# Optimization experiments

Measured on AMD Instinct MI355X. Metric: run time of the kernel, lower is better.

Reference implementation:

```python
import jax, jax.numpy as jnp
import numpy as np

# dims: n=batch, T=n_shifts, dX=16, dU=8, H=256 hidden, L=128 ldim, K=64 n_aux (L=2K)

def setup_inputs() -> dict:
    key = jax.random.key(0)
    ks = jax.random.split(key, 16)
    n, T, dX, dU, H, L, K = 64, 64, 16, 8, 256, 128, 64
    def lin(k, fan_in, shape):
        return (jax.random.uniform(k, shape, jnp.float32) * 2.0 - 1.0) / np.sqrt(fan_in)
    xs = jax.random.normal(ks[0], (n, T, dX), jnp.float32)
    us = jax.random.normal(ks[1], (n, T - 1, dU), jnp.float32)
    theta = jax.random.uniform(ks[2], (K,), jnp.float32) * (2.0 * np.pi)
    inp = {
        'xs': xs, 'us': us,
        # stacked x-aux encoders (K copies): BN affine, 3 linear layers (last no bias), output scale
        'x_gamma': jnp.ones((K, dX)), 'x_beta': jnp.zeros((K, dX)),
        'xW1': lin(ks[3], dX, (K, dX, H)), 'xb1': jnp.zeros((K, H)),
        'xW2': lin(ks[4], H, (K, H, H)), 'xb2': jnp.zeros((K, H)),
        'xW3': lin(ks[5], H, (K, H, L)), 'x_scale': jnp.ones((K, L)),
        # stacked u-aux encoders (K copies)
        'u_gamma': jnp.ones((K, dU)), 'u_beta': jnp.zeros((K, dU)),
        'uW1': lin(ks[6], dU, (K, dU, H)), 'ub1': jnp.zeros((K, H)),
        'uW2': lin(ks[7], H, (K, H, H)), 'ub2': jnp.zeros((K, H)),
        'uW3': lin(ks[8], H, (K, H, L)), 'u_scale': jnp.ones((K, L)),
        # Jordan-block complex eigenvalues (|lam| ~ 0.95)
        'reL': 0.95 * jnp.cos(theta), 'imL': 0.95 * jnp.sin(theta),
        # decoder C: Linear(ldim, dim, bias=False) -> weight [dX, L]
        'C_W': lin(ks[9], L, (dX, L)),
    }
    return inp


def _encoder(x, gamma, beta, W1, b1, W2, b2, W3, scale):
    # x: [M, D]; stacked params over K nets. BN stats (training mode) are per-feature over M,
    # identical across nets since the same x feeds every net.
    mu = x.mean(0)
    var = ((x - mu) ** 2).mean(0)
    xn = (x - mu) * jax.lax.rsqrt(var + 1e-5)          # [M, D]
    h = xn[None] * gamma[:, None, :] + beta[:, None, :]  # [K, M, D]
    h = jax.nn.leaky_relu(jnp.einsum('kmd,kdh->kmh', h, W1) + b1[:, None, :])
    h = jax.nn.leaky_relu(jnp.einsum('kmd,kdh->kmh', h, W2) + b2[:, None, :])
    h = jnp.einsum('kmd,kdh->kmh', h, W3)               # last layer: no bias
    return h * scale[:, None, :]                        # [K, M, L]


def reference(xs, us, x_gamma, x_beta, xW1, xb1, xW2, xb2, xW3, x_scale,
              u_gamma, u_beta, uW1, ub1, uW2, ub2, uW3, u_scale, reL, imL, C_W):
    n, T, dX = xs.shape
    K = reL.shape[0]
    L = 2 * K
    Tm1 = T - 1
    # phi1s: [n, T, K(net), K(pair), 2]
    phi = _encoder(xs.reshape(n * T, dX), x_gamma, x_beta, xW1, xb1, xW2, xb2, xW3, x_scale)
    phi1s = jnp.moveaxis(phi, 0, 1).reshape(n, T, K, K, 2)
    # ures = psi(u) - psi(0): [n, T-1, K, K, 2]
    uflat = us.reshape(n * Tm1, -1)
    psi_u = _encoder(uflat, u_gamma, u_beta, uW1, ub1, uW2, ub2, uW3, u_scale)
    psi_0 = _encoder(jnp.zeros_like(uflat), u_gamma, u_beta, uW1, ub1, uW2, ub2, uW3, u_scale)
    ures = jnp.moveaxis(psi_u - psi_0, 0, 1).reshape(n, Tm1, K, K, 2)
    # block-diagonal Koopman: per net j a 2x2 rotation-scale [[re, im], [-im, re]]
    R = jnp.stack([jnp.stack([reL, imL], -1), jnp.stack([-imL, reL], -1)], -2)  # [K, 2, 2]

    def step(p, u_t):
        p = jnp.einsum('bjkc,jcd->bjkd', p + u_t, R)
        return p, p

    _, preds = jax.lax.scan(step, phi1s[:, 0], jnp.moveaxis(ures, 0, 1))
    preds = jnp.moveaxis(preds, 0, 1)  # [n, T-1, K, K, 2]

    def phi2y(p):
        # sum over net axis (-3), flatten pair dims -> [.., L], decode with C
        return p.sum(-3).reshape(*p.shape[:-3], L) @ C_W.T

    y = phi2y(phi1s[:, 1:])
    y_pred = phi2y(preds)
    return y, y_pred
```

## Files before the change

kernel.cpp:

```cpp
#include <hip/hip_runtime.h>

typedef __bf16 bf16_t;
typedef __bf16 bf16x8 __attribute__((ext_vector_type(8)));
typedef __bf16 bf16x4 __attribute__((ext_vector_type(4)));
typedef float  f32x4  __attribute__((ext_vector_type(4)));

#define PHI_JS  (4096 * 128 + 64)
#define PSIU_JS (4032 * 128 + 64)

__global__ __launch_bounds__(256) void prep_all_kernel(
    const float* __restrict__ xW1, const float* __restrict__ xb1,
    const float* __restrict__ xg,  const float* __restrict__ xbeta,
    const float* __restrict__ uW1, const float* __restrict__ ub1,
    const float* __restrict__ ug,  const float* __restrict__ ubeta,
    const float* __restrict__ xW2, const float* __restrict__ uW2,
    const float* __restrict__ xW3, const float* __restrict__ uW3,
    const float* __restrict__ x_scale, const float* __restrict__ u_scale,
    const float* __restrict__ xs, const float* __restrict__ us,
    bf16_t* __restrict__ xW1t, float* __restrict__ xb1p,
    bf16_t* __restrict__ uW1t, float* __restrict__ ub1p,
    bf16_t* __restrict__ xW2t, bf16_t* __restrict__ uW2t,
    bf16_t* __restrict__ xW3t, bf16_t* __restrict__ uW3t,
    float* __restrict__ part, float* __restrict__ zout)
{
    const int t = blockIdx.x, tid = threadIdx.x;
    __shared__ float tile[32][33];
    __shared__ float h1[256], h2[256];

    if (t < 12288) {
        const float* in; bf16_t* outp; const float* scale = nullptr;
        int j, r0, c0, C;
        if (t < 8192) {
            C = 256;
            j = (t & 4095) >> 6;
            const int tl = t & 63; r0 = (tl >> 3) * 32; c0 = (tl & 7) * 32;
            if (t < 4096) { in = xW2; outp = xW2t; }
            else          { in = uW2; outp = uW2t; }
        } else {
            C = 128;
            const int l = t - 8192;
            j = (l & 2047) >> 5;
            const int tl = l & 31; r0 = (tl >> 2) * 32; c0 = (tl & 3) * 32;
            if (l < 2048) { in = xW3; outp = xW3t; scale = x_scale + j * 128; }
            else          { in = uW3; outp = uW3t; scale = u_scale + j * 128; }
        }
        const int R = 256;
        in   += (size_t)j * R * C;
        bf16_t* op = outp + (size_t)j * R * C;
        const int tx = tid & 31, ty = tid >> 5;
        #pragma unroll
        for (int i = 0; i < 4; i++)
            tile[ty + i * 8][tx] = in[(size_t)(r0 + ty + i * 8) * C + c0 + tx];
        __syncthreads();
        #pragma unroll
        for (int i = 0; i < 4; i++) {
            int c = c0 + ty + i * 8;
            float sc = scale ? scale[c] : 1.f;
            op[(size_t)c * R + r0 + tx] = (bf16_t)(tile[tx][ty + i * 8] * sc);
        }
    } else if (t < 12416) {
        const int bid = t - 12288, j = bid & 63, h = tid;
        const float *W1, *b1, *gamma, *beta; bf16_t* W1t; float* b1p; int D;
        if (bid < 64) { W1 = xW1; b1 = xb1; gamma = xg; beta = xbeta; W1t = xW1t; b1p = xb1p; D = 16; }
        else          { W1 = uW1; b1 = ub1; gamma = ug; beta = ubeta; W1t = uW1t; b1p = ub1p; D = 8; }
        float bacc = b1[j * 256 + h];
        bf16_t* orow = W1t + (size_t)(j * 256 + h) * 32;
        for (int d = 0; d < 32; d++) orow[d] = (bf16_t)0.f;
        for (int d = 0; d < D; d++) {
            float w = W1[((size_t)j * D + d) * 256 + h];
            orow[d] = (bf16_t)(gamma[j * D + d] * w);
            bacc += beta[j * D + d] * w;
        }
        b1p[j * 256 + h] = bacc;
    } else if (t < 12512) {
        const int bid = t - 12416;
        const bool isx = bid < 64;
        const float* x = isx ? xs : us;
        const int D   = isx ? 16 : 8;
        const int lb  = isx ? bid : bid - 64;
        const int per = isx ? 1024 : 1008;
        const int start = lb * per;
        float a = 0.f, b = 0.f;
        for (int idx = start + tid; idx < start + per; idx += 256) {
            float v = x[idx];
            a += v; b += v * v;
        }
        float* s1 = h1; float* s2 = h2;
        s1[tid] = a; s2[tid] = b;
        __syncthreads();
        if (tid < D) {
            float sa = 0.f, sb = 0.f;
            for (int k = tid; k < 256; k += D) { sa += s1[k]; sb += s2[k]; }
            part[bid * 32 + tid]      = sa;
            part[bid * 32 + 16 + tid] = sb;
        }
    } else {
        const int g = (t - 12512) * 256 + tid;
        for (int i = g; i < 2 * 64 * 63 * 16; i += 64 * 256)
            zout[i] = 0.f;
    }
}

__global__ __launch_bounds__(512, 4) void fused_mlp_kernel(
    const float* __restrict__ xs, const float* __restrict__ us,
    const float* __restrict__ part,
    const bf16_t* __restrict__ xW1t, const float* __restrict__ xb1p,
    const bf16_t* __restrict__ xW2t, const float* __restrict__ xb2,
    const bf16_t* __restrict__ xW3t,
    const bf16_t* __restrict__ uW1t, const float* __restrict__ ub1p,
    const bf16_t* __restrict__ uW2t, const float* __restrict__ ub2,
    const bf16_t* __restrict__ uW3t,
    const float* __restrict__ uW1r, const float* __restrict__ ub1r,
    const float* __restrict__ ubetar, const float* __restrict__ uW2r,
    const float* __restrict__ uW3r, const float* __restrict__ u_scaler,
    float* __restrict__ psi0_out,
    bf16_t* __restrict__ phi, bf16_t* __restrict__ psiu)
{
    const int bid  = blockIdx.x;
    const int tid  = threadIdx.x;

    __shared__ __align__(16) bf16_t hs[128 * 256];
    __shared__ float stats_s[32];

    if (bid >= 4096) {
        const int j = bid - 4096;
        float* fb  = (float*)hs;
        float* h1  = fb;
        float* h2  = fb + 256;
        float* tmp = fb + 512;
        const int h = tid & 255, half = tid >> 8;
        if (half == 0) {
            float bacc = ub1r[j * 256 + h];
            #pragma unroll
            for (int d = 0; d < 8; d++)
                bacc += ubetar[j * 8 + d] * uW1r[((size_t)j * 8 + d) * 256 + h];
            h1[h] = fmaxf(bacc, 0.01f * bacc);
        }
        __syncthreads();
        {
            float acc = (half == 0) ? ub2[j * 256 + h] : 0.f;
            const float* w2 = uW2r + (size_t)j * 65536 + (size_t)half * 128 * 256 + h;
            #pragma unroll 16
            for (int d = 0; d < 128; d++) acc += h1[half * 128 + d] * w2[(size_t)d * 256];
            tmp[tid] = acc;
        }
        __syncthreads();
        if (half == 0) {
            float v = tmp[h] + tmp[h + 256];
            h2[h] = fmaxf(v, 0.01f * v);
        }
        __syncthreads();
        {
            const int h3 = tid & 127, qd = tid >> 7;
            float acc = 0.f;
            const float* w3 = uW3r + (size_t)j * 32768 + (size_t)qd * 64 * 128 + h3;
            #pragma unroll 16
            for (int d = 0; d < 64; d++) acc += h2[qd * 64 + d] * w3[(size_t)d * 128];
            tmp[tid] = acc;
        }
        __syncthreads();
        if (tid < 128)
            psi0_out[j * 128 + tid] =
                (tmp[tid] + tmp[tid + 128] + tmp[tid + 256] + tmp[tid + 384])
                * u_scaler[j * 128 + tid];
        return;
    }

    const int xcd  = bid & 7;
    const int slot = bid >> 3;
    const int band = slot >> 6;
    const int t64  = slot & 63;
    const int j    = xcd * 8 + band;
    const bool is_x = t64 < 32;
    const int tile  = is_x ? t64 : (t64 - 32);

    const float*  In  = is_x ? xs   : us;
    const int     D   = is_x ? 16   : 8;
    const bf16_t* W1t = is_x ? xW1t : uW1t;
    const float*  b1p = is_x ? xb1p : ub1p;
    const bf16_t* W2t = is_x ? xW2t : uW2t;
    const float*  b2  = is_x ? xb2  : ub2;
    const bf16_t* W3t = is_x ? xW3t : uW3t;
    bf16_t* outp      = is_x ? phi  : psiu;
    const int M       = is_x ? 4096 : 4032;
    const size_t JS   = is_x ? (size_t)PHI_JS : (size_t)PSIU_JS;

    const int row0 = tile * 128;
    const int wave = tid >> 6;
    const int lane = tid & 63;
    const int quad = lane >> 4;
    const int l16  = lane & 15;
    const int lo2  = l16 & 3, hi2 = l16 >> 2;

    if (tid < 16) {
        if (is_x) {
            float sa = 0.f, sb = 0.f;
            #pragma unroll 8
            for (int b = 0; b < 64; b++) { sa += part[b * 32 + tid]; sb += part[b * 32 + 16 + tid]; }
            float mu = sa / 4096.f, var = sb / 4096.f - mu * mu;
            stats_s[tid] = mu; stats_s[16 + tid] = rsqrtf(var + 1e-5f);
        } else if (tid < 8) {
            float sa = 0.f, sb = 0.f;
            #pragma unroll 8
            for (int b = 64; b < 96; b++) { sa += part[b * 32 + tid]; sb += part[b * 32 + 16 + tid]; }
            float mu = sa / 4032.f, var = sb / 4032.f - mu * mu;
            stats_s[tid] = mu; stats_s[16 + tid] = rsqrtf(var + 1e-5f);
        }
    }
    __syncthreads();

    const f32x4 vzero = {0.f, 0.f, 0.f, 0.f};

    char* const hsB = (char*)hs;
    const char* const abase = hsB + l16 * 512 + ((quad ^ lo2) << 4);
    const int  wlow0 = (quad >> 1) ^ lo2;
    char* const wbase = hsB + l16 * 512 + ((wave ^ hi2) << 6) + ((quad & 1) << 3);

    {
        bf16x8 wfr[2];
        #pragma unroll
        for (int nbi = 0; nbi < 2; nbi++)
            wfr[nbi] = *reinterpret_cast<const bf16x8*>(
                W1t + (size_t)(j * 256 + wave * 32 + nbi * 16 + l16) * 32 + quad * 8);

        f32x4 acc[8][2];
        #pragma unroll
        for (int a = 0; a < 8; a++) { acc[a][0] = vzero; acc[a][1] = vzero; }

        const int c0 = quad * 8;
        #pragma unroll
        for (int mb = 0; mb < 8; mb++) {
            bf16x8 a;
            if (c0 < D) {
                int row = row0 + mb * 16 + l16;
                if (row > M - 1) row = M - 1;
                const float* xp = In + (size_t)row * D + c0;
                f32x4 v0 = *reinterpret_cast<const f32x4*>(xp);
                f32x4 v1 = *reinterpret_cast<const f32x4*>(xp + 4);
                #pragma unroll
                for (int e = 0; e < 4; e++) a[e]     = (bf16_t)((v0[e] - stats_s[c0 + e])     * stats_s[16 + c0 + e]);
                #pragma unroll
                for (int e = 0; e < 4; e++) a[4 + e] = (bf16_t)((v1[e] - stats_s[c0 + 4 + e]) * stats_s[16 + c0 + 4 + e]);
            } else {
                #pragma unroll
                for (int e = 0; e < 8; e++) a[e] = (bf16_t)0.f;
            }
            #pragma unroll
            for (int nbi = 0; nbi < 2; nbi++)
                acc[mb][nbi] = __builtin_amdgcn_mfma_f32_16x16x32_bf16(
                    wfr[nbi], a, acc[mb][nbi], 0, 0, 0);
        }

        #pragma unroll
        for (int nbi = 0; nbi < 2; nbi++) {
            const f32x4 bias = *reinterpret_cast<const f32x4*>(
                b1p + j * 256 + wave * 32 + nbi * 16 + quad * 4);
            char* wp = wbase + ((wlow0 ^ (nbi << 1)) << 4);
            #pragma unroll
            for (int mb = 0; mb < 8; mb++) {
                bf16x4 pk;
                #pragma unroll
                for (int r = 0; r < 4; r++) {
                    float v = acc[mb][nbi][r] + bias[r];
                    v = fmaxf(v, 0.01f * v);
                    pk[r] = (bf16_t)v;
                }
                *reinterpret_cast<bf16x4*>(wp + mb * 8192) = pk;
            }
        }
    }
    __syncthreads();

    {
        f32x4 acc[8][2];
        #pragma unroll
        for (int a = 0; a < 8; a++) { acc[a][0] = vzero; acc[a][1] = vzero; }

        const bf16_t* w2base = W2t + ((size_t)j * 256 + wave * 32 + l16) * 256 + quad * 8;

        bf16x8 wr[3][2];
        #pragma unroll
        for (int d = 0; d < 3; d++)
            #pragma unroll
            for (int nbi = 0; nbi < 2; nbi++)
                wr[d][nbi] = *reinterpret_cast<const bf16x8*>(w2base + nbi * 4096 + d * 32);

        #pragma unroll
        for (int kk = 0; kk < 8; kk++) {
            const int c = kk % 3;
            const char* ap = abase + ((kk ^ hi2) << 6);
            bf16x8 av0[4];
            #pragma unroll
            for (int mb = 0; mb < 4; mb++)
                av0[mb] = *reinterpret_cast<const bf16x8*>(ap + mb * 8192);
            #pragma unroll
            for (int nbi = 0; nbi < 2; nbi++)
                #pragma unroll
                for (int mb = 0; mb < 4; mb++)
                    acc[mb][nbi] = __builtin_amdgcn_mfma_f32_16x16x32_bf16(
                        wr[c][nbi], av0[mb], acc[mb][nbi], 0, 0, 0);
            bf16x8 av1[4];
            #pragma unroll
            for (int mb = 0; mb < 4; mb++)
                av1[mb] = *reinterpret_cast<const bf16x8*>(ap + (mb + 4) * 8192);
            #pragma unroll
            for (int nbi = 0; nbi < 2; nbi++)
                #pragma unroll
                for (int mb = 4; mb < 8; mb++)
                    acc[mb][nbi] = __builtin_amdgcn_mfma_f32_16x16x32_bf16(
                        wr[c][nbi], av1[mb - 4], acc[mb][nbi], 0, 0, 0);
            if (kk < 5) {
                #pragma unroll
                for (int nbi = 0; nbi < 2; nbi++)
                    wr[c][nbi] = *reinterpret_cast<const bf16x8*>(
                        w2base + nbi * 4096 + (kk + 3) * 32);
            }
        }
        __syncthreads();
        #pragma unroll
        for (int nbi = 0; nbi < 2; nbi++) {
            const f32x4 bias = *reinterpret_cast<const f32x4*>(
                b2 + j * 256 + wave * 32 + nbi * 16 + quad * 4);
            char* wp = wbase + ((wlow0 ^ (nbi << 1)) << 4);
            #pragma unroll
            for (int mb = 0; mb < 8; mb++) {
                bf16x4 pk;
                #pragma unroll
                for (int r = 0; r < 4; r++) {
                    float v = acc[mb][nbi][r] + bias[r];
                    v = fmaxf(v, 0.01f * v);
                    pk[r] = (bf16_t)v;
                }
                *reinterpret_cast<bf16x4*>(wp + mb * 8192) = pk;
            }
        }
    }
    __syncthreads();

    {
        f32x4 acc[8];
        #pragma unroll
        for (int a = 0; a < 8; a++) acc[a] = vzero;

        const bf16_t* w3base = W3t + ((size_t)j * 128 + wave * 16 + l16) * 256 + quad * 8;

        bf16x8 wr[3];
        #pragma unroll
        for (int d = 0; d < 3; d++)
            wr[d] = *reinterpret_cast<const bf16x8*>(w3base + d * 32);

        #pragma unroll
        for (int kk = 0; kk < 8; kk++) {
            const int c = kk % 3;
            const char* ap = abase + ((kk ^ hi2) << 6);
            bf16x8 av0[4];
            #pragma unroll
            for (int mb = 0; mb < 4; mb++)
                av0[mb] = *reinterpret_cast<const bf16x8*>(ap + mb * 8192);
            #pragma unroll
            for (int mb = 0; mb < 4; mb++)
                acc[mb] = __builtin_amdgcn_mfma_f32_16x16x32_bf16(
                    wr[c], av0[mb], acc[mb], 0, 0, 0);
            bf16x8 av1[4];
            #pragma unroll
            for (int mb = 0; mb < 4; mb++)
                av1[mb] = *reinterpret_cast<const bf16x8*>(ap + (mb + 4) * 8192);
            #pragma unroll
            for (int mb = 4; mb < 8; mb++)
                acc[mb] = __builtin_amdgcn_mfma_f32_16x16x32_bf16(
                    wr[c], av1[mb - 4], acc[mb], 0, 0, 0);
            if (kk < 5)
                wr[c] = *reinterpret_cast<const bf16x8*>(w3base + (kk + 3) * 32);
        }
        __syncthreads();
        {
            const int sp3 = (wave * 2 + (quad >> 1)) ^ l16;
            char* w3p = hsB + l16 * 256 + sp3 * 16 + ((quad & 1) << 3);
            #pragma unroll
            for (int mb = 0; mb < 8; mb++) {
                bf16x4 pk;
                #pragma unroll
                for (int r = 0; r < 4; r++) pk[r] = (bf16_t)acc[mb][r];
                *reinterpret_cast<bf16x4*>(w3p + mb * 4096) = pk;
            }
        }
    }
    __syncthreads();
    #pragma unroll
    for (int p = 0; p < 4; p++) {
        const int rr = p * 32 + (tid >> 4);
        const int s  = tid & 15;
        if (row0 + rr < M) {
            bf16x8 v = *reinterpret_cast<const bf16x8*>(hs + rr * 128 + (s ^ (rr & 15)) * 8);
            *reinterpret_cast<bf16x8*>(outp + (size_t)j * JS + (size_t)(row0 + rr) * 128 + s * 8) = v;
        }
    }
}

__global__ __launch_bounds__(512) void scan_kernel(
    const bf16_t* __restrict__ phi, const bf16_t* __restrict__ psiu,
    const float* __restrict__ psi0, const float* __restrict__ reL,
    const float* __restrict__ imL, const float* __restrict__ C_W,
    float* __restrict__ y, float* __restrict__ ypred) {
    const int b = blockIdx.x >> 3, jg = blockIdx.x & 7;
    const int tid = threadIdx.x;
    const int wave = tid >> 6, lane = tid & 63;
    __shared__ float redP[2][8][128];
    __shared__ float redY[2][8][128];
    __shared__ float SPb[8][132];
    __shared__ float SYb[8][132];
    __shared__ float CsT[2048];
    #pragma unroll
    for (int i = 0; i < 4; i++) {
        const int idx = tid + i * 512;
        CsT[(idx & 127) * 16 + (idx >> 7)] = C_W[idx];
    }

    const int j0 = jg * 8 + wave;
    float sx, sy, p0x, p0y, lre, lim;
    {
        unsigned v = *reinterpret_cast<const unsigned*>(
            phi + (size_t)j0 * PHI_JS + (size_t)(b * 64) * 128 + lane * 2);
        sx = __uint_as_float(v << 16); sy = __uint_as_float(v & 0xFFFF0000u);
        float2 p0 = *reinterpret_cast<const float2*>(psi0 + j0 * 128 + lane * 2);
        p0x = p0.x; p0y = p0.y;
        lre = reL[j0]; lim = imL[j0];
    }
    const bf16_t* up = psiu + (size_t)j0 * PSIU_JS + (size_t)(b * 63) * 128 + lane * 2;
    const bf16_t* pp = phi  + (size_t)j0 * PHI_JS  + (size_t)(b * 64 + 1) * 128 + lane * 2;
    unsigned cu0 = *reinterpret_cast<const unsigned*>(up);
    unsigned cp0 = *reinterpret_cast<const unsigned*>(pp);
    unsigned nu1 = *reinterpret_cast<const unsigned*>(up + 128);
    unsigned np1 = *reinterpret_cast<const unsigned*>(pp + 128);

    const int ds  = (tid >> 7) & 1;
    const int dr  = tid & 127;
    const int dtt = dr >> 4, doo = dr & 15;

    int tbase = 0;
    for (int t = 0; t < 63; t++) {
        unsigned nu2 = 0, np2 = 0;
        if (t < 61) {
            nu2 = *reinterpret_cast<const unsigned*>(up + (t + 2) * 128);
            np2 = *reinterpret_cast<const unsigned*>(pp + (t + 2) * 128);
        }
        float px = sx + (__uint_as_float(cu0 << 16) - p0x);
        float py = sy + (__uint_as_float(cu0 & 0xFFFF0000u) - p0y);
        sx = px * lre - py * lim;
        sy = px * lim + py * lre;
        const float yx = __uint_as_float(cp0 << 16);
        const float yy = __uint_as_float(cp0 & 0xFFFF0000u);
        const int db = t & 1;
        redP[db][wave][lane * 2]     = sx;
        redP[db][wave][lane * 2 + 1] = sy;
        redY[db][wave][lane * 2]     = yx;
        redY[db][wave][lane * 2 + 1] = yy;
        __syncthreads();
        const int slot = t & 7;
        if (tid < 128) {
            SPb[slot][tid] =
                redP[db][0][tid] + redP[db][1][tid] + redP[db][2][tid] + redP[db][3][tid]
              + redP[db][4][tid] + redP[db][5][tid] + redP[db][6][tid] + redP[db][7][tid];
        } else if (tid < 256) {
            const int tl = tid - 128;
            SYb[slot][tl] =
                redY[db][0][tl] + redY[db][1][tl] + redY[db][2][tl] + redY[db][3][tl]
              + redY[db][4][tl] + redY[db][5][tl] + redY[db][6][tl] + redY[db][7][tl];
        }
        cu0 = nu1; cp0 = np1; nu1 = nu2; np1 = np2;
        if (slot == 7 || t == 62) {
            __syncthreads();
            if (tid < 256 && dtt <= slot) {
                const float* S = ds ? SYb[dtt] : SPb[dtt];
                float acc = 0.f;
                #pragma unroll
                for (int i = 0; i < 128; i++) acc += S[i] * CsT[i * 16 + doo];
                float* dst = ds ? (y     + (b * 63 + tbase + dtt) * 16 + doo)
                                : (ypred + (b * 63 + tbase + dtt) * 16 + doo);
                atomicAdd(dst, acc);
            }
            __syncthreads();
            tbase = t + 1;
        }
    }
}

extern "C" void kernel_launch(void* const* d_in, const int* in_sizes, int n_in,
                              void* d_out, int out_size, void* d_ws, size_t ws_size,
                              hipStream_t stream) {
    const float* xs      = (const float*)d_in[0];
    const float* us      = (const float*)d_in[1];
    const float* x_gamma = (const float*)d_in[2];
    const float* x_beta  = (const float*)d_in[3];
    const float* xW1     = (const float*)d_in[4];
    const float* xb1     = (const float*)d_in[5];
    const float* xW2     = (const float*)d_in[6];
    const float* xb2     = (const float*)d_in[7];
    const float* xW3     = (const float*)d_in[8];
    const float* x_scale = (const float*)d_in[9];
    const float* u_gamma = (const float*)d_in[10];
    const float* u_beta  = (const float*)d_in[11];
    const float* uW1     = (const float*)d_in[12];
    const float* ub1     = (const float*)d_in[13];
    const float* uW2     = (const float*)d_in[14];
    const float* ub2     = (const float*)d_in[15];
    const float* uW3     = (const float*)d_in[16];
    const float* u_scale = (const float*)d_in[17];
    const float* reL     = (const float*)d_in[18];
    const float* imL     = (const float*)d_in[19];
    const float* C_W     = (const float*)d_in[20];

    char* ws = (char*)d_ws;
    size_t off = 0;
    auto alloc = [&](size_t bytes) -> char* {
        char* p = ws + off;
        off += (bytes + 255) & ~(size_t)255;
        return p;
    };
    float*  part = (float*)alloc(96 * 32 * 4);
    bf16_t* xW1t = (bf16_t*)alloc((size_t)64 * 256 * 32 * 2);
    float*  xb1p = (float*) alloc((size_t)64 * 256 * 4);
    bf16_t* xW2t = (bf16_t*)alloc((size_t)64 * 256 * 256 * 2);
    bf16_t* xW3t = (bf16_t*)alloc((size_t)64 * 128 * 256 * 2);
    bf16_t* uW1t = (bf16_t*)alloc((size_t)64 * 256 * 32 * 2);
    float*  ub1p = (float*) alloc((size_t)64 * 256 * 4);
    bf16_t* uW2t = (bf16_t*)alloc((size_t)64 * 256 * 256 * 2);
    bf16_t* uW3t = (bf16_t*)alloc((size_t)64 * 128 * 256 * 2);
    float*  psi0 = (float*) alloc((size_t)64 * 128 * 4);
    bf16_t* phi  = (bf16_t*)alloc((size_t)64 * PHI_JS  * 2);
    bf16_t* psiu = (bf16_t*)alloc((size_t)64 * PSIU_JS * 2);

    float* y_out     = (float*)d_out;
    float* ypred_out = y_out + 64 * 63 * 16;

    prep_all_kernel<<<12576, 256, 0, stream>>>(
        xW1, xb1, x_gamma, x_beta, uW1, ub1, u_gamma, u_beta,
        xW2, uW2, xW3, uW3, x_scale, u_scale, xs, us,
        xW1t, xb1p, uW1t, ub1p, xW2t, uW2t, xW3t, uW3t, part, y_out);
    fused_mlp_kernel<<<4160, 512, 0, stream>>>(
        xs, us, part,
        xW1t, xb1p, xW2t, xb2, xW3t, uW1t, ub1p, uW2t, ub2, uW3t,
        uW1, ub1, u_beta, uW2, uW3, u_scale, psi0,
        phi, psiu);
    scan_kernel<<<512, 512, 0, stream>>>(
        phi, psiu, psi0, reL, imL, C_W, y_out, ypred_out);
}
```

Baseline: 343.9 us.

## Split scan time range across two blocks with recomputed prefix state

The scan kernel's 63 time steps are split into two halves handled by separate blocks, doubling the grid to 1024. The second-half block first replays the recurrence over the first 32 steps in registers, without any reductions or decoding, to rebuild its starting state. It then runs the usual reduce and decode loop only for its own steps. This shortens the serial critical path and raises occupancy, at the cost of redundant recurrence work and extra reads of psiu.

```diff
diff --git a/kernel.cpp b/kernel.cpp
--- a/kernel.cpp
+++ b/kernel.cpp
@@ -402,7 +402,10 @@
     const float* __restrict__ psi0, const float* __restrict__ reL,
     const float* __restrict__ imL, const float* __restrict__ C_W,
     float* __restrict__ y, float* __restrict__ ypred) {
-    const int b = blockIdx.x >> 3, jg = blockIdx.x & 7;
+    const int bid = blockIdx.x;
+    const int th = bid & 1;
+    const int jg = (bid >> 1) & 7;
+    const int b  = bid >> 4;
     const int tid = threadIdx.x;
     const int wave = tid >> 6, lane = tid & 63;
     __shared__ float redP[2][8][128];
@@ -416,6 +419,9 @@
         CsT[(idx & 127) * 16 + (idx >> 7)] = C_W[idx];
     }
 
+    const int tb = th * 32;
+    const int te = th ? 63 : 32;
+
     const int j0 = jg * 8 + wave;
     float sx, sy, p0x, p0y, lre, lim;
     {
@@ -428,17 +434,35 @@
     }
     const bf16_t* up = psiu + (size_t)j0 * PSIU_JS + (size_t)(b * 63) * 128 + lane * 2;
     const bf16_t* pp = phi  + (size_t)j0 * PHI_JS  + (size_t)(b * 64 + 1) * 128 + lane * 2;
-    unsigned cu0 = *reinterpret_cast<const unsigned*>(up);
-    unsigned cp0 = *reinterpret_cast<const unsigned*>(pp);
-    unsigned nu1 = *reinterpret_cast<const unsigned*>(up + 128);
-    unsigned np1 = *reinterpret_cast<const unsigned*>(pp + 128);
+
+    unsigned cu0 = *reinterpret_cast<const unsigned*>(up + tb * 128);
+    unsigned cp0 = *reinterpret_cast<const unsigned*>(pp + tb * 128);
+    unsigned nu1 = *reinterpret_cast<const unsigned*>(up + (tb + 1) * 128);
+    unsigned np1 = *reinterpret_cast<const unsigned*>(pp + (tb + 1) * 128);
+
+    if (th) {
+        #pragma unroll
+        for (int c = 0; c < 2; c++) {
+            unsigned buf[16];
+            #pragma unroll
+            for (int i = 0; i < 16; i++)
+                buf[i] = *reinterpret_cast<const unsigned*>(up + (c * 16 + i) * 128);
+            #pragma unroll
+            for (int i = 0; i < 16; i++) {
+                float px = sx + (__uint_as_float(buf[i] << 16) - p0x);
+                float py = sy + (__uint_as_float(buf[i] & 0xFFFF0000u) - p0y);
+                sx = px * lre - py * lim;
+                sy = px * lim + py * lre;
+            }
+        }
+    }
 
     const int ds  = (tid >> 7) & 1;
     const int dr  = tid & 127;
     const int dtt = dr >> 4, doo = dr & 15;
 
-    int tbase = 0;
-    for (int t = 0; t < 63; t++) {
+    int tbase = tb;
+    for (int t = tb; t < te; t++) {
         unsigned nu2 = 0, np2 = 0;
         if (t < 61) {
             nu2 = *reinterpret_cast<const unsigned*>(up + (t + 2) * 128);
@@ -456,7 +480,7 @@
         redY[db][wave][lane * 2]     = yx;
         redY[db][wave][lane * 2 + 1] = yy;
         __syncthreads();
-        const int slot = t & 7;
+        const int slot = (t - tb) & 7;
         if (tid < 128) {
             SPb[slot][tid] =
                 redP[db][0][tid] + redP[db][1][tid] + redP[db][2][tid] + redP[db][3][tid]
@@ -468,7 +492,7 @@
               + redY[db][4][tl] + redY[db][5][tl] + redY[db][6][tl] + redY[db][7][tl];
         }
         cu0 = nu1; cp0 = np1; nu1 = nu2; np1 = np2;
-        if (slot == 7 || t == 62) {
+        if (slot == 7 || t == te - 1) {
             __syncthreads();
             if (tid < 256 && dtt <= slot) {
                 const float* S = ds ? SYb[dtt] : SPb[dtt];
@@ -542,6 +566,6 @@
         xW1t, xb1p, xW2t, xb2, xW3t, uW1t, ub1p, uW2t, ub2, uW3t,
         uW1, ub1, u_beta, uW2, uW3, u_scale, psi0,
         phi, psiu);
-    scan_kernel<<<512, 512, 0, stream>>>(
+    scan_kernel<<<1024, 512, 0, stream>>>(
         phi, psiu, psi0, reL, imL, C_W, y_out, ypred_out);
 }
```

Result: faster. 335.0 us (-2.6%).

## Remap scan threads so net reduction uses wave shuffles instead of per-step barriers

Applied to the files above, without the earlier changes.

The scan kernel now maps 8 networks into one wave (lane>>3) and 8 pair columns per lane group, so summing over networks becomes an in-wave xor-shuffle reduction instead of a shared-memory reduction with a barrier every time step. Barriers now occur only once per 8-step chunk. Loads are batched 8 steps at a time in double-buffered registers and the loop is fully unrolled. The trade-off is more shuffle instructions, higher register pressure from the unrolled buffers, and less coalesced global loads, since each lane now reads a different network's stride.

```diff
diff --git a/kernel.cpp b/kernel.cpp
--- a/kernel.cpp
+++ b/kernel.cpp
@@ -405,8 +405,9 @@
     const int b = blockIdx.x >> 3, jg = blockIdx.x & 7;
     const int tid = threadIdx.x;
     const int wave = tid >> 6, lane = tid & 63;
-    __shared__ float redP[2][8][128];
-    __shared__ float redY[2][8][128];
+    const int net_sub = lane >> 3;
+    const int p_lo = lane & 7;
+    const int pair = wave * 8 + p_lo;
     __shared__ float SPb[8][132];
     __shared__ float SYb[8][132];
     __shared__ float CsT[2048];
@@ -415,73 +416,82 @@
         const int idx = tid + i * 512;
         CsT[(idx & 127) * 16 + (idx >> 7)] = C_W[idx];
     }
-
-    const int j0 = jg * 8 + wave;
+    __syncthreads();
+
+    const int j0 = jg * 8 + net_sub;
     float sx, sy, p0x, p0y, lre, lim;
     {
         unsigned v = *reinterpret_cast<const unsigned*>(
-            phi + (size_t)j0 * PHI_JS + (size_t)(b * 64) * 128 + lane * 2);
+            phi + (size_t)j0 * PHI_JS + (size_t)(b * 64) * 128 + pair * 2);
         sx = __uint_as_float(v << 16); sy = __uint_as_float(v & 0xFFFF0000u);
-        float2 p0 = *reinterpret_cast<const float2*>(psi0 + j0 * 128 + lane * 2);
+        float2 p0 = *reinterpret_cast<const float2*>(psi0 + j0 * 128 + pair * 2);
         p0x = p0.x; p0y = p0.y;
         lre = reL[j0]; lim = imL[j0];
     }
-    const bf16_t* up = psiu + (size_t)j0 * PSIU_JS + (size_t)(b * 63) * 128 + lane * 2;
-    const bf16_t* pp = phi  + (size_t)j0 * PHI_JS  + (size_t)(b * 64 + 1) * 128 + lane * 2;
-    unsigned cu0 = *reinterpret_cast<const unsigned*>(up);
-    unsigned cp0 = *reinterpret_cast<const unsigned*>(pp);
-    unsigned nu1 = *reinterpret_cast<const unsigned*>(up + 128);
-    unsigned np1 = *reinterpret_cast<const unsigned*>(pp + 128);
+    const bf16_t* up = psiu + (size_t)j0 * PSIU_JS + (size_t)(b * 63) * 128 + pair * 2;
+    const bf16_t* pp = phi  + (size_t)j0 * PHI_JS  + (size_t)(b * 64 + 1) * 128 + pair * 2;
 
     const int ds  = (tid >> 7) & 1;
     const int dr  = tid & 127;
     const int dtt = dr >> 4, doo = dr & 15;
-
-    int tbase = 0;
-    for (int t = 0; t < 63; t++) {
-        unsigned nu2 = 0, np2 = 0;
-        if (t < 61) {
-            nu2 = *reinterpret_cast<const unsigned*>(up + (t + 2) * 128);
-            np2 = *reinterpret_cast<const unsigned*>(pp + (t + 2) * 128);
-        }
-        float px = sx + (__uint_as_float(cu0 << 16) - p0x);
-        float py = sy + (__uint_as_float(cu0 & 0xFFFF0000u) - p0y);
-        sx = px * lre - py * lim;
-        sy = px * lim + py * lre;
-        const float yx = __uint_as_float(cp0 << 16);
-        const float yy = __uint_as_float(cp0 & 0xFFFF0000u);
-        const int db = t & 1;
-        redP[db][wave][lane * 2]     = sx;
-        redP[db][wave][lane * 2 + 1] = sy;
-        redY[db][wave][lane * 2]     = yx;
-        redY[db][wave][lane * 2 + 1] = yy;
-        __syncthreads();
-        const int slot = t & 7;
-        if (tid < 128) {
-            SPb[slot][tid] =
-                redP[db][0][tid] + redP[db][1][tid] + redP[db][2][tid] + redP[db][3][tid]
-              + redP[db][4][tid] + redP[db][5][tid] + redP[db][6][tid] + redP[db][7][tid];
-        } else if (tid < 256) {
-            const int tl = tid - 128;
-            SYb[slot][tl] =
-                redY[db][0][tl] + redY[db][1][tl] + redY[db][2][tl] + redY[db][3][tl]
-              + redY[db][4][tl] + redY[db][5][tl] + redY[db][6][tl] + redY[db][7][tl];
-        }
-        cu0 = nu1; cp0 = np1; nu1 = nu2; np1 = np2;
-        if (slot == 7 || t == 62) {
-            __syncthreads();
-            if (tid < 256 && dtt <= slot) {
-                const float* S = ds ? SYb[dtt] : SPb[dtt];
-                float acc = 0.f;
-                #pragma unroll
-                for (int i = 0; i < 128; i++) acc += S[i] * CsT[i * 16 + doo];
-                float* dst = ds ? (y     + (b * 63 + tbase + dtt) * 16 + doo)
-                                : (ypred + (b * 63 + tbase + dtt) * 16 + doo);
-                atomicAdd(dst, acc);
-            }
-            __syncthreads();
-            tbase = t + 1;
-        }
+    const int pcol = pair * 2;
+
+    unsigned ub[2][8], pb[2][8];
+    #pragma unroll
+    for (int i = 0; i < 8; i++) {
+        ub[0][i] = *reinterpret_cast<const unsigned*>(up + i * 128);
+        pb[0][i] = *reinterpret_cast<const unsigned*>(pp + i * 128);
+    }
+
+    #pragma unroll
+    for (int c = 0; c < 8; c++) {
+        const int cb = c & 1;
+        if (c < 7) {
+            #pragma unroll
+            for (int i = 0; i < 8; i++) {
+                const int tn = (c + 1) * 8 + i;
+                if (tn < 63) {
+                    ub[cb ^ 1][i] = *reinterpret_cast<const unsigned*>(up + tn * 128);
+                    pb[cb ^ 1][i] = *reinterpret_cast<const unsigned*>(pp + tn * 128);
+                }
+            }
+        }
+        const int n = (c == 7) ? 7 : 8;
+        #pragma unroll
+        for (int i = 0; i < 8; i++) {
+            if (i < n) {
+                const unsigned u = ub[cb][i];
+                float px = sx + (__uint_as_float(u << 16) - p0x);
+                float py = sy + (__uint_as_float(u & 0xFFFF0000u) - p0y);
+                sx = px * lre - py * lim;
+                sy = px * lim + py * lre;
+                const unsigned ph = pb[cb][i];
+                float rx = sx, ry = sy;
+                float yx = __uint_as_float(ph << 16);
+                float yy = __uint_as_float(ph & 0xFFFF0000u);
+                rx += __shfl_xor(rx, 8);  ry += __shfl_xor(ry, 8);
+                yx += __shfl_xor(yx, 8);  yy += __shfl_xor(yy, 8);
+                rx += __shfl_xor(rx, 16); ry += __shfl_xor(ry, 16);
+                yx += __shfl_xor(yx, 16); yy += __shfl_xor(yy, 16);
+                rx += __shfl_xor(rx, 32); ry += __shfl_xor(ry, 32);
+                yx += __shfl_xor(yx, 32); yy += __shfl_xor(yy, 32);
+                if (net_sub < 2) {
+                    SPb[i][pcol + net_sub] = net_sub ? ry : rx;
+                    SYb[i][pcol + net_sub] = net_sub ? yy : yx;
+                }
+            }
+        }
+        __syncthreads();
+        if (tid < 256 && dtt < n) {
+            const float* S = ds ? SYb[dtt] : SPb[dtt];
+            float acc = 0.f;
+            #pragma unroll
+            for (int i = 0; i < 128; i++) acc += S[i] * CsT[i * 16 + doo];
+            float* dst = ds ? (y     + (b * 63 + c * 8 + dtt) * 16 + doo)
+                            : (ypred + (b * 63 + c * 8 + dtt) * 16 + doo);
+            atomicAdd(dst, acc);
+        }
+        __syncthreads();
     }
 }
 
```

New measurement: 353.3 us. 1.03x slower.
